# Kernel optimization log

Hardware: AMD Instinct MI355X
Metric: run time of the kernel (lower is better)

## Reference

```python
import jax, jax.numpy as jnp
import numpy as np
from jax.scipy.special import logsumexp

B, S, H, L = 64, 512, 1024, 9  # batch, seq_len, hidden_size, num_labels


def setup_inputs() -> dict:
    key = jax.random.key(0)
    ks = jax.random.split(key, 6)
    inputs = jax.random.normal(ks[0], (B, S, H), jnp.float32)
    labels = jax.random.randint(ks[1], (B, S), 0, L).astype(jnp.int64)
    mask = jnp.ones((B, S), jnp.int32)
    # fc parameters (nn.Linear(hidden_size, num_labels))
    W = jax.random.normal(ks[2], (L, H), jnp.float32) / np.sqrt(H)
    b = jnp.zeros((L,), jnp.float32)
    # CRF parameters (include_start_end_trans=True)
    trans_m = jax.random.normal(ks[3], (L, L), jnp.float32) * 0.1
    start_scores = jax.random.normal(ks[4], (L,), jnp.float32) * 0.1
    end_scores = jax.random.normal(ks[5], (L,), jnp.float32) * 0.1
    return dict(inputs=inputs, labels=labels, mask=mask, W=W, b=b,
                trans_m=trans_m, start_scores=start_scores, end_scores=end_scores)


def _crf_nll_mean(inputs, W, b, trans_m, start_scores, end_scores, labels, mask):
    # logits = fc(inputs): [B, S, L]
    logits = jnp.einsum('bsh,lh->bsl', inputs, W) + b
    feats = jnp.swapaxes(logits, 0, 1)           # [S, B, L] (fastNLP transposes)
    tags = jnp.swapaxes(labels, 0, 1)            # [S, B]
    m = jnp.swapaxes(mask, 0, 1).astype(feats.dtype)  # [S, B]
    seq_len, batch, n_tags = feats.shape

    # ---- log-partition via forward algorithm (lax.scan over time) ----
    alpha0 = feats[0] + start_scores[None, :]    # [B, L]

    def step(alpha, x):
        emit, mt = x                              # emit: [B, L], mt: [B]
        # tmp[b, i, j] = alpha[b, i] + trans_m[i, j] + emit[b, j]
        tmp = alpha[:, :, None] + trans_m[None, :, :] + emit[:, None, :]
        new = logsumexp(tmp, axis=1)              # [B, L]
        alpha = jnp.where(mt[:, None] > 0, new, alpha)
        return alpha, None

    alpha, _ = jax.lax.scan(step, alpha0, (feats[1:], m[1:]))
    norm = logsumexp(alpha + end_scores[None, :], axis=1)   # [B]

    # ---- gold path score ----
    emit = jnp.take_along_axis(feats, tags[:, :, None], axis=2)[:, :, 0] * m  # [S, B]
    trans = trans_m[tags[:-1], tags[1:]] * m[1:]                               # [S-1, B]
    score = emit.sum(0) + trans.sum(0)                                         # [B]
    last_idx = m.sum(0).astype(jnp.int32) - 1                                  # [B]
    last_tags = tags[last_idx, jnp.arange(batch)]
    score = score + start_scores[tags[0]] + end_scores[last_tags]

    # loss = crf(logits, labels, mask).mean()
    return jnp.mean(norm - score)


def reference(inputs, labels, mask, W, b, trans_m, start_scores, end_scores):
    return _crf_nll_mean(inputs, W, b, trans_m, start_scores, end_scores, labels, mask)
```

## Files before the change

### kernel.cpp

```cpp
#include <hip/hip_runtime.h>


#define BATCH 64
#define SEQ   512
#define HID   1024
#define NLAB  9
#define CHUNK 32
#define NCHUNK (SEQ / CHUNK)
#define NREC (BATCH * NCHUNK * NLAB)

__device__ __forceinline__ float exp2_fast(float x) { return __builtin_amdgcn_exp2f(x); }
__device__ __forceinline__ float log2_fast(float x) { return __builtin_amdgcn_logf(x); }

#define LOG2E 1.4426950408889634f
#define LN2   0.6931471805599453f

__global__ __launch_bounds__(256) void logits_kernel(
    const float* __restrict__ inp, const float* __restrict__ Wg,
    const float* __restrict__ bias, float* __restrict__ feats)
{
    __shared__ float Wl[NLAB * 1056];
    const int tid = threadIdx.x;
    for (int i = tid; i < NLAB * HID; i += 256) {
        int l = i >> 10, col = i & 1023;
        Wl[l * 1056 + col + (col >> 5)] = Wg[i];
    }
    __syncthreads();

    const int lane = tid & 63;
    const int wv   = tid >> 6;
    const int p    = lane & 15;
    const int g    = lane >> 4;
    const long row0 = (long)blockIdx.x * 64 + wv * 16 + g * 4;

    const float* r = inp + row0 * HID;
    float acc[4][NLAB];
    #pragma unroll
    for (int rr = 0; rr < 4; ++rr)
        #pragma unroll
        for (int l = 0; l < NLAB; ++l) acc[rr][l] = 0.f;

    #pragma unroll
    for (int c = 0; c < 4; ++c) {
        const int col0 = c * 256 + p * 16;
        const int sk = col0 + (col0 >> 5);
        float xs[4][16];
        #pragma unroll
        for (int rr = 0; rr < 4; ++rr) {
            const float* rp = r + (long)rr * HID + col0;
            #pragma unroll
            for (int q = 0; q < 4; ++q)
                ((float4*)xs[rr])[q] = ((const float4*)rp)[q];
        }
        #pragma unroll
        for (int l = 0; l < NLAB; ++l) {
            const float* wp = &Wl[l * 1056 + sk];
            float w[16];
            #pragma unroll
            for (int q = 0; q < 4; ++q)
                ((float4*)w)[q] = ((const float4*)wp)[q];
            #pragma unroll
            for (int rr = 0; rr < 4; ++rr) {
                float a = acc[rr][l];
                #pragma unroll
                for (int k = 0; k < 16; ++k) a = fmaf(xs[rr][k], w[k], a);
                acc[rr][l] = a;
            }
        }
    }

    #pragma unroll
    for (int rr = 0; rr < 4; ++rr)
        #pragma unroll
        for (int l = 0; l < NLAB; ++l) {
            float a = acc[rr][l];
            a += __shfl_xor(a, 8, 64);
            a += __shfl_xor(a, 4, 64);
            a += __shfl_xor(a, 2, 64);
            a += __shfl_xor(a, 1, 64);
            acc[rr][l] = a;
        }
    if (p == 0) {
        #pragma unroll
        for (int rr = 0; rr < 4; ++rr) {
            float* o = feats + (row0 + rr) * NLAB;
            #pragma unroll
            for (int l = 0; l < NLAB; ++l)
                o[l] = (acc[rr][l] + bias[l]) * LOG2E;
        }
    }
}

__global__ __launch_bounds__(64) void chunk_kernel(
    const float* __restrict__ feats, const float* __restrict__ trans,
    const int* __restrict__ mask, float* __restrict__ P,
    float* __restrict__ out)
{
    const int lane = threadIdx.x;
    if (blockIdx.x == 0 && lane == 63) out[0] = 0.0f;
    const int g = lane / 9;
    const int j = lane - g * 9;
    int rid = blockIdx.x * 7 + g;
    bool act = (g < 7) && (rid < NREC);
    if (!act) rid = 0;

    const int i  = rid % NLAB;
    const int bc = rid / NLAB;
    const int c  = bc & (NCHUNK - 1);
    const int b  = bc >> 4;

    float tr[NLAB];
    #pragma unroll
    for (int k = 0; k < NLAB; ++k) tr[k] = trans[k * NLAB + j] * LOG2E;
    const float tri = trans[i * NLAB + j] * LOG2E;

    const float* fb = feats + (long)b * SEQ * NLAB;
    const int* mb = mask + b * SEQ;
    const int ts = (c == 0) ? 1 : c * CHUNK;
    const int te = (c + 1) * CHUNK;
    const int sbase = g * 9;

    float a;
    {
        int m0 = mb[ts];
        float e0 = fb[ts * NLAB + j];
        float aid = (i == j) ? 0.0f : -1e30f;
        a = (m0 > 0) ? (tri + e0) : aid;
    }

    float e_nxt = fb[(ts + 1) * NLAB + j];
    int   m_nxt = mb[ts + 1];
    for (int t = ts + 1; t < te; ++t) {
        float e = e_nxt;
        int  mt = m_nxt;
        if (t + 1 < te) {
            e_nxt = fb[(t + 1) * NLAB + j];
            m_nxt = mb[t + 1];
        }
        float v[NLAB];
        #pragma unroll
        for (int k = 0; k < NLAB; ++k) v[k] = __shfl(a, sbase + k, 64) + tr[k];
        float m01 = fmaxf(v[0], v[1]), m23 = fmaxf(v[2], v[3]);
        float m45 = fmaxf(v[4], v[5]), m67 = fmaxf(v[6], v[7]);
        float mx = fmaxf(fmaxf(fmaxf(m01, m23), fmaxf(m45, m67)), v[8]);
        float s = 0.0f;
        #pragma unroll
        for (int k = 0; k < NLAB; ++k) s += exp2_fast(v[k] - mx);
        float an = mx + log2_fast(s) + e;
        a = (mt > 0) ? an : a;
    }
    if (act) P[(long)rid * NLAB + j] = a;
}

__global__ __launch_bounds__(64) void final_kernel(
    const float* __restrict__ feats, const float* __restrict__ trans,
    const float* __restrict__ startv, const float* __restrict__ endv,
    const int* __restrict__ labels, const int* __restrict__ mask,
    const float* __restrict__ P, float* __restrict__ out)
{
    const int b = blockIdx.x, lane = threadIdx.x;
    const float* fb = feats + (long)b * SEQ * NLAB;
    const int* lb = labels + b * SEQ;
    const int* mb = mask + b * SEQ;

    float gsum = 0.0f; int msum = 0;
    for (int t = lane; t < SEQ; t += 64) {
        int tag = lb[t];
        int mt = mb[t];
        if (mt > 0) {
            gsum += fb[t * NLAB + tag];
            msum++;
            if (t > 0) gsum += trans[lb[t - 1] * NLAB + tag] * LOG2E;
        }
    }
    #pragma unroll
    for (int off = 32; off > 0; off >>= 1) {
        gsum += __shfl_xor(gsum, off, 64);
        msum += __shfl_xor(msum, off, 64);
    }

    const int j = lane % 9;
    float al = fb[j] + startv[j] * LOG2E;
    const float* Pb = P + (long)b * NCHUNK * 81;
    float pc[NLAB];
    #pragma unroll
    for (int i = 0; i < NLAB; ++i) pc[i] = Pb[i * NLAB + j];
    #pragma unroll
    for (int c = 0; c < NCHUNK; ++c) {
        float pn[NLAB];
        if (c < NCHUNK - 1) {
            #pragma unroll
            for (int i = 0; i < NLAB; ++i) pn[i] = Pb[(c + 1) * 81 + i * NLAB + j];
        } else {
            #pragma unroll
            for (int i = 0; i < NLAB; ++i) pn[i] = 0.0f;
        }
        float v[NLAB];
        #pragma unroll
        for (int i = 0; i < NLAB; ++i) v[i] = __shfl(al, i, 64) + pc[i];
        float m01 = fmaxf(v[0], v[1]), m23 = fmaxf(v[2], v[3]);
        float m45 = fmaxf(v[4], v[5]), m67 = fmaxf(v[6], v[7]);
        float mx = fmaxf(fmaxf(fmaxf(m01, m23), fmaxf(m45, m67)), v[8]);
        float s = 0.0f;
        #pragma unroll
        for (int i = 0; i < NLAB; ++i) s += exp2_fast(v[i] - mx);
        al = mx + log2_fast(s);
        #pragma unroll
        for (int i = 0; i < NLAB; ++i) pc[i] = pn[i];
    }
    al += endv[j] * LOG2E;

    float v[NLAB];
    #pragma unroll
    for (int i = 0; i < NLAB; ++i) v[i] = __shfl(al, i, 64);
    float m01 = fmaxf(v[0], v[1]), m23 = fmaxf(v[2], v[3]);
    float m45 = fmaxf(v[4], v[5]), m67 = fmaxf(v[6], v[7]);
    float mx = fmaxf(fmaxf(fmaxf(m01, m23), fmaxf(m45, m67)), v[8]);
    float s = 0.0f;
    #pragma unroll
    for (int i = 0; i < NLAB; ++i) s += exp2_fast(v[i] - mx);
    float norm = mx + log2_fast(s);

    if (lane == 0) {
        int li = (msum > 0) ? (msum - 1) : 0;
        float score = gsum + startv[lb[0]] * LOG2E + endv[lb[li]] * LOG2E;
        atomicAdd(out, (norm - score) * (LN2 / (float)BATCH));
    }
}

extern "C" void kernel_launch(void* const* d_in, const int* in_sizes, int n_in,
                              void* d_out, int out_size, void* d_ws, size_t ws_size,
                              hipStream_t stream)
{
    const float* inp    = (const float*)d_in[0];
    const int*   labels = (const int*)d_in[1];
    const int*   mask   = (const int*)d_in[2];
    const float* W      = (const float*)d_in[3];
    const float* bias   = (const float*)d_in[4];
    const float* trans  = (const float*)d_in[5];
    const float* startv = (const float*)d_in[6];
    const float* endv   = (const float*)d_in[7];

    float* feats = (float*)d_ws;
    float* P     = feats + BATCH * SEQ * NLAB;
    float* out   = (float*)d_out;

    hipLaunchKernelGGL(logits_kernel, dim3(BATCH * SEQ / 64), dim3(256), 0, stream,
                       inp, W, bias, feats);
    hipLaunchKernelGGL(chunk_kernel, dim3((NREC + 6) / 7), dim3(64), 0, stream,
                       feats, trans, mask, P, out);
    hipLaunchKernelGGL(final_kernel, dim3(BATCH), dim3(64), 0, stream,
                       feats, trans, startv, endv, labels, mask, P, out);
}
```

Before: 236.0 us.

## Fuse logits GEMV with per-chunk CRF scan and gold-score partials

Merges the logits kernel and the chunk-scan kernel into one kernel. Each block computes emissions for one (batch, chunk) of 32 timesteps into shared memory, then runs the chunked forward recursion and the gold-path partial sums from LDS. This removes the global feats round-trip and one launch, and moves the gold-score reduction out of the final kernel. The trade-off is twice as many blocks, each reloading W into LDS, with only two wavefronts doing the serial scan while the rest idle.

Measured after the change: 242.5 us. +2.8%, slower.

```diff
diff --git a/kernel.cpp b/kernel.cpp
--- a/kernel.cpp
+++ b/kernel.cpp
@@ -7,7 +7,6 @@
 #define NLAB  9
 #define CHUNK 32
 #define NCHUNK (SEQ / CHUNK)
-#define NREC (BATCH * NCHUNK * NLAB)
 
 __device__ __forceinline__ float exp2_fast(float x) { return __builtin_amdgcn_exp2f(x); }
 __device__ __forceinline__ float log2_fast(float x) { return __builtin_amdgcn_logf(x); }
@@ -15,12 +14,23 @@
 #define LOG2E 1.4426950408889634f
 #define LN2   0.6931471805599453f
 
-__global__ __launch_bounds__(256) void logits_kernel(
+__global__ __launch_bounds__(256) void fused_kernel(
     const float* __restrict__ inp, const float* __restrict__ Wg,
-    const float* __restrict__ bias, float* __restrict__ feats)
+    const float* __restrict__ bias, const float* __restrict__ trans,
+    const int* __restrict__ labels, const int* __restrict__ mask,
+    float* __restrict__ P, float* __restrict__ a0buf,
+    float* __restrict__ goldpart, float* __restrict__ msumpart,
+    float* __restrict__ out)
 {
     __shared__ float Wl[NLAB * 1056];
+    __shared__ float em[CHUNK][NLAB];
     const int tid = threadIdx.x;
+    if (blockIdx.x == 0 && tid == 255) out[0] = 0.0f;
+
+    const int b = blockIdx.x >> 4;
+    const int c = blockIdx.x & (NCHUNK - 1);
+    const int t0 = c * CHUNK;
+
     for (int i = tid; i < NLAB * HID; i += 256) {
         int l = i >> 10, col = i & 1023;
         Wl[l * 1056 + col + (col >> 5)] = Wg[i];
@@ -30,23 +40,22 @@
     const int lane = tid & 63;
     const int wv   = tid >> 6;
     const int p    = lane & 15;
-    const int g    = lane >> 4;
-    const long row0 = (long)blockIdx.x * 64 + wv * 16 + g * 4;
-
-    const float* r = inp + row0 * HID;
-    float acc[4][NLAB];
-    #pragma unroll
-    for (int rr = 0; rr < 4; ++rr)
+    const int gg   = wv * 4 + (lane >> 4);
+    const float* r = inp + ((long)b * SEQ + t0 + 2 * gg) * HID;
+
+    float acc[2][NLAB];
+    #pragma unroll
+    for (int rr = 0; rr < 2; ++rr)
         #pragma unroll
         for (int l = 0; l < NLAB; ++l) acc[rr][l] = 0.f;
 
     #pragma unroll
-    for (int c = 0; c < 4; ++c) {
-        const int col0 = c * 256 + p * 16;
+    for (int c4 = 0; c4 < 4; ++c4) {
+        const int col0 = c4 * 256 + p * 16;
         const int sk = col0 + (col0 >> 5);
-        float xs[4][16];
-        #pragma unroll
-        for (int rr = 0; rr < 4; ++rr) {
+        float xs[2][16];
+        #pragma unroll
+        for (int rr = 0; rr < 2; ++rr) {
             const float* rp = r + (long)rr * HID + col0;
             #pragma unroll
             for (int q = 0; q < 4; ++q)
@@ -60,7 +69,7 @@
             for (int q = 0; q < 4; ++q)
                 ((float4*)w)[q] = ((const float4*)wp)[q];
             #pragma unroll
-            for (int rr = 0; rr < 4; ++rr) {
+            for (int rr = 0; rr < 2; ++rr) {
                 float a = acc[rr][l];
                 #pragma unroll
                 for (int k = 0; k < 16; ++k) a = fmaf(xs[rr][k], w[k], a);
@@ -68,9 +77,8 @@
             }
         }
     }
-
-    #pragma unroll
-    for (int rr = 0; rr < 4; ++rr)
+    #pragma unroll
+    for (int rr = 0; rr < 2; ++rr)
         #pragma unroll
         for (int l = 0; l < NLAB; ++l) {
             float a = acc[rr][l];
@@ -82,105 +90,101 @@
         }
     if (p == 0) {
         #pragma unroll
-        for (int rr = 0; rr < 4; ++rr) {
-            float* o = feats + (row0 + rr) * NLAB;
+        for (int rr = 0; rr < 2; ++rr)
             #pragma unroll
             for (int l = 0; l < NLAB; ++l)
-                o[l] = (acc[rr][l] + bias[l]) * LOG2E;
-        }
+                em[2 * gg + rr][l] = (acc[rr][l] + bias[l]) * LOG2E;
+    }
+    __syncthreads();
+
+    const int* mb = mask + b * SEQ;
+    const int* lb = labels + b * SEQ;
+
+    if (wv == 0) {
+        float gp = 0.f, ms = 0.f;
+        if (lane < CHUNK) {
+            int t = t0 + lane;
+            int mt = mb[t];
+            if (mt > 0) {
+                int tag = lb[t];
+                gp = em[lane][tag];
+                ms = 1.f;
+                if (t > 0) gp += trans[lb[t - 1] * NLAB + tag] * LOG2E;
+            }
+        }
+        #pragma unroll
+        for (int off = 32; off > 0; off >>= 1) {
+            gp += __shfl_xor(gp, off, 64);
+            ms += __shfl_xor(ms, off, 64);
+        }
+        if (lane == 0) {
+            goldpart[b * NCHUNK + c] = gp;
+            msumpart[b * NCHUNK + c] = ms;
+        }
+    } else if (wv <= 2) {
+        const int g9 = lane / 9;
+        const int j  = lane - g9 * 9;
+        const bool act = (wv == 1) ? (g9 < 7) : (g9 < 2);
+        const int i = (wv == 1) ? g9 : 7 + g9;
+        const int sbase = g9 * 9;
+
+        float tr[NLAB];
+        #pragma unroll
+        for (int k = 0; k < NLAB; ++k) tr[k] = trans[k * NLAB + j] * LOG2E;
+        const int isafe = act ? i : 0;
+        const float tri = trans[isafe * NLAB + j] * LOG2E;
+
+        const int ts = (c == 0) ? 1 : t0;
+        const int te = t0 + CHUNK;
+
+        float a;
+        {
+            int m0 = mb[ts];
+            float e0 = em[ts - t0][j];
+            float aid = (isafe == j) ? 0.0f : -1e30f;
+            a = (m0 > 0) ? (tri + e0) : aid;
+        }
+        int m_nxt = mb[ts + 1];
+        for (int t = ts + 1; t < te; ++t) {
+            int mt = m_nxt;
+            if (t + 1 < te) m_nxt = mb[t + 1];
+            float e = em[t - t0][j];
+            float v[NLAB];
+            #pragma unroll
+            for (int k = 0; k < NLAB; ++k) v[k] = __shfl(a, sbase + k, 64) + tr[k];
+            float m01 = fmaxf(v[0], v[1]), m23 = fmaxf(v[2], v[3]);
+            float m45 = fmaxf(v[4], v[5]), m67 = fmaxf(v[6], v[7]);
+            float mx = fmaxf(fmaxf(fmaxf(m01, m23), fmaxf(m45, m67)), v[8]);
+            float s = 0.0f;
+            #pragma unroll
+            for (int k = 0; k < NLAB; ++k) s += exp2_fast(v[k] - mx);
+            float an = mx + log2_fast(s) + e;
+            a = (mt > 0) ? an : a;
+        }
+        if (act) P[(long)((b * NCHUNK + c) * NLAB + i) * NLAB + j] = a;
+    } else {
+        if (c == 0 && lane < NLAB) a0buf[b * NLAB + lane] = em[0][lane];
     }
 }
 
-__global__ __launch_bounds__(64) void chunk_kernel(
-    const float* __restrict__ feats, const float* __restrict__ trans,
-    const int* __restrict__ mask, float* __restrict__ P,
-    float* __restrict__ out)
-{
-    const int lane = threadIdx.x;
-    if (blockIdx.x == 0 && lane == 63) out[0] = 0.0f;
-    const int g = lane / 9;
-    const int j = lane - g * 9;
-    int rid = blockIdx.x * 7 + g;
-    bool act = (g < 7) && (rid < NREC);
-    if (!act) rid = 0;
-
-    const int i  = rid % NLAB;
-    const int bc = rid / NLAB;
-    const int c  = bc & (NCHUNK - 1);
-    const int b  = bc >> 4;
-
-    float tr[NLAB];
-    #pragma unroll
-    for (int k = 0; k < NLAB; ++k) tr[k] = trans[k * NLAB + j] * LOG2E;
-    const float tri = trans[i * NLAB + j] * LOG2E;
-
-    const float* fb = feats + (long)b * SEQ * NLAB;
-    const int* mb = mask + b * SEQ;
-    const int ts = (c == 0) ? 1 : c * CHUNK;
-    const int te = (c + 1) * CHUNK;
-    const int sbase = g * 9;
-
-    float a;
-    {
-        int m0 = mb[ts];
-        float e0 = fb[ts * NLAB + j];
-        float aid = (i == j) ? 0.0f : -1e30f;
-        a = (m0 > 0) ? (tri + e0) : aid;
-    }
-
-    float e_nxt = fb[(ts + 1) * NLAB + j];
-    int   m_nxt = mb[ts + 1];
-    for (int t = ts + 1; t < te; ++t) {
-        float e = e_nxt;
-        int  mt = m_nxt;
-        if (t + 1 < te) {
-            e_nxt = fb[(t + 1) * NLAB + j];
-            m_nxt = mb[t + 1];
-        }
-        float v[NLAB];
-        #pragma unroll
-        for (int k = 0; k < NLAB; ++k) v[k] = __shfl(a, sbase + k, 64) + tr[k];
-        float m01 = fmaxf(v[0], v[1]), m23 = fmaxf(v[2], v[3]);
-        float m45 = fmaxf(v[4], v[5]), m67 = fmaxf(v[6], v[7]);
-        float mx = fmaxf(fmaxf(fmaxf(m01, m23), fmaxf(m45, m67)), v[8]);
-        float s = 0.0f;
-        #pragma unroll
-        for (int k = 0; k < NLAB; ++k) s += exp2_fast(v[k] - mx);
-        float an = mx + log2_fast(s) + e;
-        a = (mt > 0) ? an : a;
-    }
-    if (act) P[(long)rid * NLAB + j] = a;
-}
-
 __global__ __launch_bounds__(64) void final_kernel(
-    const float* __restrict__ feats, const float* __restrict__ trans,
     const float* __restrict__ startv, const float* __restrict__ endv,
-    const int* __restrict__ labels, const int* __restrict__ mask,
-    const float* __restrict__ P, float* __restrict__ out)
+    const int* __restrict__ labels, const float* __restrict__ P,
+    const float* __restrict__ a0buf, const float* __restrict__ goldpart,
+    const float* __restrict__ msumpart, float* __restrict__ out)
 {
     const int b = blockIdx.x, lane = threadIdx.x;
-    const float* fb = feats + (long)b * SEQ * NLAB;
-    const int* lb = labels + b * SEQ;
-    const int* mb = mask + b * SEQ;
-
-    float gsum = 0.0f; int msum = 0;
-    for (int t = lane; t < SEQ; t += 64) {
-        int tag = lb[t];
-        int mt = mb[t];
-        if (mt > 0) {
-            gsum += fb[t * NLAB + tag];
-            msum++;
-            if (t > 0) gsum += trans[lb[t - 1] * NLAB + tag] * LOG2E;
-        }
-    }
+
+    float gp = (lane < NCHUNK) ? goldpart[b * NCHUNK + lane] : 0.f;
+    float ms = (lane < NCHUNK) ? msumpart[b * NCHUNK + lane] : 0.f;
     #pragma unroll
     for (int off = 32; off > 0; off >>= 1) {
-        gsum += __shfl_xor(gsum, off, 64);
-        msum += __shfl_xor(msum, off, 64);
+        gp += __shfl_xor(gp, off, 64);
+        ms += __shfl_xor(ms, off, 64);
     }
 
     const int j = lane % 9;
-    float al = fb[j] + startv[j] * LOG2E;
+    float al = a0buf[b * NLAB + j] + startv[j] * LOG2E;
     const float* Pb = P + (long)b * NCHUNK * 81;
     float pc[NLAB];
     #pragma unroll
@@ -222,8 +226,10 @@
     float norm = mx + log2_fast(s);
 
     if (lane == 0) {
+        const int* lb = labels + b * SEQ;
+        int msum = (int)ms;
         int li = (msum > 0) ? (msum - 1) : 0;
-        float score = gsum + startv[lb[0]] * LOG2E + endv[lb[li]] * LOG2E;
+        float score = gp + startv[lb[0]] * LOG2E + endv[lb[li]] * LOG2E;
         atomicAdd(out, (norm - score) * (LN2 / (float)BATCH));
     }
 }
@@ -241,14 +247,15 @@
     const float* startv = (const float*)d_in[6];
     const float* endv   = (const float*)d_in[7];
 
-    float* feats = (float*)d_ws;
-    float* P     = feats + BATCH * SEQ * NLAB;
-    float* out   = (float*)d_out;
-
-    hipLaunchKernelGGL(logits_kernel, dim3(BATCH * SEQ / 64), dim3(256), 0, stream,
-                       inp, W, bias, feats);
-    hipLaunchKernelGGL(chunk_kernel, dim3((NREC + 6) / 7), dim3(64), 0, stream,
-                       feats, trans, mask, P, out);
+    float* P        = (float*)d_ws;
+    float* a0buf    = P + BATCH * NCHUNK * 81;
+    float* goldpart = a0buf + BATCH * NLAB;
+    float* msumpart = goldpart + BATCH * NCHUNK;
+    float* out      = (float*)d_out;
+
+    hipLaunchKernelGGL(fused_kernel, dim3(BATCH * NCHUNK), dim3(256), 0, stream,
+                       inp, W, bias, trans, labels, mask,
+                       P, a0buf, goldpart, msumpart, out);
     hipLaunchKernelGGL(final_kernel, dim3(BATCH), dim3(64), 0, stream,
-                       feats, trans, startv, endv, labels, mask, P, out);
+                       startv, endv, labels, P, a0buf, goldpart, msumpart, out);
 }
```

## Compute logits with bf16 MFMA instead of fp32 FMA with LDS weights

Applied to the files above, without the earlier changes.

Replaces the scalar fp32 FMA projection, which staged weights in shared memory, with bf16 MFMA 16x16x32 instructions. A new kernel pre-converts W to bf16, scales it by log2(e), and pads it to 16 labels. Inputs are converted to bf16 in registers before each MFMA, so the projection runs on the matrix cores with no LDS staging. This lowers matmul precision to bf16 and adds one extra small kernel launch.

After: 237.6 us. Within noise of the previous version (+0.7%).

```diff
diff --git a/kernel.cpp b/kernel.cpp
--- a/kernel.cpp
+++ b/kernel.cpp
@@ -1,4 +1,5 @@
 #include <hip/hip_runtime.h>
+#include <hip/hip_bf16.h>
 
 
 #define BATCH 64
@@ -8,6 +9,8 @@
 #define CHUNK 32
 #define NCHUNK (SEQ / CHUNK)
 #define NREC (BATCH * NCHUNK * NLAB)
+#define NROWS (BATCH * SEQ)
+#define NTILES (NROWS / 16)
 
 __device__ __forceinline__ float exp2_fast(float x) { return __builtin_amdgcn_exp2f(x); }
 __device__ __forceinline__ float log2_fast(float x) { return __builtin_amdgcn_logf(x); }
@@ -15,78 +18,65 @@
 #define LOG2E 1.4426950408889634f
 #define LN2   0.6931471805599453f
 
+typedef __attribute__((ext_vector_type(8))) short short8;
+typedef __attribute__((ext_vector_type(4))) float float4v;
+
+__global__ __launch_bounds__(256) void wcvt_kernel(
+    const float* __restrict__ W, __hip_bfloat16* __restrict__ wbf)
+{
+    int idx = blockIdx.x * 256 + threadIdx.x;
+    int n = idx >> 10, k = idx & 1023;
+    float v = (n < NLAB) ? W[n * HID + k] * LOG2E : 0.0f;
+    wbf[idx] = __float2bfloat16(v);
+}
+
 __global__ __launch_bounds__(256) void logits_kernel(
-    const float* __restrict__ inp, const float* __restrict__ Wg,
+    const float* __restrict__ inp, const __hip_bfloat16* __restrict__ wbf,
     const float* __restrict__ bias, float* __restrict__ feats)
 {
-    __shared__ float Wl[NLAB * 1056];
-    const int tid = threadIdx.x;
-    for (int i = tid; i < NLAB * HID; i += 256) {
-        int l = i >> 10, col = i & 1023;
-        Wl[l * 1056 + col + (col >> 5)] = Wg[i];
-    }
-    __syncthreads();
-
-    const int lane = tid & 63;
-    const int wv   = tid >> 6;
-    const int p    = lane & 15;
-    const int g    = lane >> 4;
-    const long row0 = (long)blockIdx.x * 64 + wv * 16 + g * 4;
-
-    const float* r = inp + row0 * HID;
-    float acc[4][NLAB];
-    #pragma unroll
-    for (int rr = 0; rr < 4; ++rr)
-        #pragma unroll
-        for (int l = 0; l < NLAB; ++l) acc[rr][l] = 0.f;
-
-    #pragma unroll
-    for (int c = 0; c < 4; ++c) {
-        const int col0 = c * 256 + p * 16;
-        const int sk = col0 + (col0 >> 5);
-        float xs[4][16];
-        #pragma unroll
-        for (int rr = 0; rr < 4; ++rr) {
-            const float* rp = r + (long)rr * HID + col0;
-            #pragma unroll
-            for (int q = 0; q < 4; ++q)
-                ((float4*)xs[rr])[q] = ((const float4*)rp)[q];
-        }
-        #pragma unroll
-        for (int l = 0; l < NLAB; ++l) {
-            const float* wp = &Wl[l * 1056 + sk];
-            float w[16];
-            #pragma unroll
-            for (int q = 0; q < 4; ++q)
-                ((float4*)w)[q] = ((const float4*)wp)[q];
-            #pragma unroll
-            for (int rr = 0; rr < 4; ++rr) {
-                float a = acc[rr][l];
-                #pragma unroll
-                for (int k = 0; k < 16; ++k) a = fmaf(xs[rr][k], w[k], a);
-                acc[rr][l] = a;
-            }
-        }
-    }
-
-    #pragma unroll
-    for (int rr = 0; rr < 4; ++rr)
-        #pragma unroll
-        for (int l = 0; l < NLAB; ++l) {
-            float a = acc[rr][l];
-            a += __shfl_xor(a, 8, 64);
-            a += __shfl_xor(a, 4, 64);
-            a += __shfl_xor(a, 2, 64);
-            a += __shfl_xor(a, 1, 64);
-            acc[rr][l] = a;
-        }
-    if (p == 0) {
-        #pragma unroll
-        for (int rr = 0; rr < 4; ++rr) {
-            float* o = feats + (row0 + rr) * NLAB;
-            #pragma unroll
-            for (int l = 0; l < NLAB; ++l)
-                o[l] = (acc[rr][l] + bias[l]) * LOG2E;
+    const int lane = threadIdx.x & 63;
+    const int wv   = threadIdx.x >> 6;
+    const int wid  = blockIdx.x * 4 + wv;
+    const int n    = lane & 15;
+    const int q8   = lane >> 4;
+    const long r0  = (long)wid * 32;
+
+    const float* a0p = inp + (r0 + n) * HID + q8 * 8;
+    const float* a1p = a0p + 16 * HID;
+    const short* bp  = (const short*)wbf + n * HID + q8 * 8;
+
+    float4v acc0 = {0.f, 0.f, 0.f, 0.f};
+    float4v acc1 = {0.f, 0.f, 0.f, 0.f};
+
+    for (int kk = 0; kk < 32; ++kk) {
+        const int ko = kk * 32;
+        float x0[8], x1[8];
+        *(float4*)(x0)     = *(const float4*)(a0p + ko);
+        *(float4*)(x0 + 4) = *(const float4*)(a0p + ko + 4);
+        *(float4*)(x1)     = *(const float4*)(a1p + ko);
+        *(float4*)(x1 + 4) = *(const float4*)(a1p + ko + 4);
+        short8 bfrag = *(const short8*)(bp + ko);
+
+        short8 af0, af1;
+        #pragma unroll
+        for (int j = 0; j < 8; ++j) {
+            union { __hip_bfloat16 h; short s; } u0, u1;
+            u0.h = __float2bfloat16(x0[j]);
+            u1.h = __float2bfloat16(x1[j]);
+            af0[j] = u0.s;
+            af1[j] = u1.s;
+        }
+        acc0 = __builtin_amdgcn_mfma_f32_16x16x32_bf16(af0, bfrag, acc0, 0, 0, 0);
+        acc1 = __builtin_amdgcn_mfma_f32_16x16x32_bf16(af1, bfrag, acc1, 0, 0, 0);
+    }
+
+    if (n < NLAB) {
+        const float bK = bias[n] * LOG2E;
+        #pragma unroll
+        for (int r = 0; r < 4; ++r) {
+            const long row = r0 + q8 * 4 + r;
+            feats[row * NLAB + n]        = acc0[r] + bK;
+            feats[(row + 16) * NLAB + n] = acc1[r] + bK;
         }
     }
 }
@@ -242,11 +232,13 @@
     const float* endv   = (const float*)d_in[7];
 
     float* feats = (float*)d_ws;
-    float* P     = feats + BATCH * SEQ * NLAB;
+    float* P     = feats + (long)NROWS * NLAB;
+    __hip_bfloat16* wbf = (__hip_bfloat16*)(P + (long)BATCH * NCHUNK * 81);
     float* out   = (float*)d_out;
 
-    hipLaunchKernelGGL(logits_kernel, dim3(BATCH * SEQ / 64), dim3(256), 0, stream,
-                       inp, W, bias, feats);
+    hipLaunchKernelGGL(wcvt_kernel, dim3(64), dim3(256), 0, stream, W, wbf);
+    hipLaunchKernelGGL(logits_kernel, dim3(NTILES / 8), dim3(256), 0, stream,
+                       inp, wbf, bias, feats);
     hipLaunchKernelGGL(chunk_kernel, dim3((NREC + 6) / 7), dim3(64), 0, stream,
                        feats, trans, mask, P, out);
     hipLaunchKernelGGL(final_kernel, dim3(BATCH), dim3(64), 0, stream,
```
